# Kernel tuning notes

Hardware: AMD Instinct MI355X
Metric: run time of the kernel (lower is better)

The kernel has to match this reference:

```python
import jax, jax.numpy as jnp
import numpy as np

N_USER = 100000
N_RECIPE = 50000
E = 1000000
H = 128


def setup_inputs() -> dict:
    key = jax.random.key(0)
    ks = jax.random.split(key, 5)
    z_user = jax.random.normal(ks[0], (N_USER, H), dtype=jnp.float32)
    z_recipe = jax.random.normal(ks[1], (N_RECIPE, H), dtype=jnp.float32)
    edge_label_index = jax.random.randint(ks[2], (2, E), 0, N_RECIPE, dtype=jnp.int64)
    W1 = jax.random.normal(ks[3], (2 * H, H), dtype=jnp.float32) * (1.0 / np.sqrt(2 * H))
    b1 = jnp.zeros((H,), dtype=jnp.float32)
    W2 = jax.random.normal(ks[4], (H, 1), dtype=jnp.float32) * (1.0 / np.sqrt(H))
    b2 = jnp.zeros((1,), dtype=jnp.float32)
    return {"z_user": z_user, "z_recipe": z_recipe,
            "edge_label_index": edge_label_index,
            "W1": W1, "b1": b1, "W2": W2, "b2": b2}


def reference(z_user, z_recipe, edge_label_index, W1, b1, W2, b2):
    row, col = edge_label_index[0], edge_label_index[1]
    # gather + concat: [E, 2H]
    z = jnp.concatenate([z_user[row], z_recipe[col]], axis=-1)
    h = jax.nn.relu(z @ W1 + b1)        # [E, H]
    out = h @ W2 + b2                    # [E, 1]
    return out.reshape(-1)
```

## Files before the change

kernel.cpp:

```cpp
#include <hip/hip_runtime.h>
#include <hip/hip_bf16.h>


#define HDIM 128

typedef __attribute__((ext_vector_type(8))) __bf16 bf16x8;
typedef __attribute__((ext_vector_type(16))) float f32x16;

static __device__ __forceinline__ unsigned short bf16_bits(float x) {
  return __builtin_bit_cast(unsigned short, static_cast<__bf16>(x));
}

static __device__ __forceinline__ float bf2f(unsigned short u) {
  return __builtin_bit_cast(float, ((unsigned int)u) << 16);
}

static __device__ __forceinline__ bf16x8 cvt8(float4 a, float4 b) {
  bf16x8 r;
  r[0] = static_cast<__bf16>(a.x);
  r[1] = static_cast<__bf16>(a.y);
  r[2] = static_cast<__bf16>(a.z);
  r[3] = static_cast<__bf16>(a.w);
  r[4] = static_cast<__bf16>(b.x);
  r[5] = static_cast<__bf16>(b.y);
  r[6] = static_cast<__bf16>(b.z);
  r[7] = static_cast<__bf16>(b.w);
  return r;
}

__global__ void prep_w1(const float* __restrict__ W1,
                        unsigned short* __restrict__ W1bf) {
  const int tid = threadIdx.x;
#pragma unroll
  for (int it = 0; it < 8; ++it) {
    const int idx = (blockIdx.x << 11) + (it << 8) + tid;
    const int k = idx >> 7;
    const int n = idx & 127;
    const int kc = k >> 4;
    const int q = (k >> 3) & 1;
    const int j = k & 7;
    const int nt = n >> 5;
    const int ln = (q << 5) | (n & 31);
    W1bf[((((kc << 2) + nt) << 6) | ln) * 8 + j] = bf16_bits(W1[idx]);
  }
}

__global__ __launch_bounds__(256, 4) void proj_nodes(
    const float* __restrict__ zu, int NU, const float* __restrict__ zr, int NR,
    const float* __restrict__ W1, const unsigned short* __restrict__ W1bf,
    unsigned short* __restrict__ Hu, unsigned short* __restrict__ Hr,
    int ublocks) {
  __shared__ unsigned short Bsw[16384];
  const int tid = threadIdx.x;
  const bool isU = (int)blockIdx.x < ublocks;
  const int kc0 = isU ? 0 : 8;

  if (W1bf) {
    const uint4* s4 = (const uint4*)(W1bf + (kc0 << 11));
    uint4* d4 = (uint4*)Bsw;
#pragma unroll
    for (int i = 0; i < 8; ++i) d4[(i << 8) + tid] = s4[(i << 8) + tid];
  } else {
    const int n = tid & 127;
    const int kh = tid >> 7;
    const int nt = n >> 5;
    const int nl = n & 31;
#pragma unroll 8
    for (int it = 0; it < 64; ++it) {
      const int kl = 2 * it + kh;
      const float w = W1[(kc0 * 16 + kl) * HDIM + n];
      const int kc = kl >> 4;
      const int q = (kl >> 3) & 1;
      const int j = kl & 7;
      const int ln = (q << 5) | nl;
      Bsw[((((kc << 2) + nt) << 6) | ln) * 8 + j] = bf16_bits(w);
    }
  }
  __syncthreads();

  const int lane = tid & 63;
  const int wid = tid >> 6;
  const int m = lane & 31;
  const int half = lane >> 5;
  const int koff = half * 8;

  const int tl = (isU ? (int)blockIdx.x : (int)blockIdx.x - ublocks) * 4 + wid;
  const int ntype = isU ? ((NU + 31) >> 5) : ((NR + 31) >> 5);
  if (tl >= ntype) return;

  const int base = tl << 5;
  const int nmax = isU ? NU : NR;
  int node = base + m;
  if (node >= nmax) node = nmax - 1;
  const float* src = (isU ? zu : zr) + (size_t)node * HDIM + koff;

  f32x16 acc[4];
#pragma unroll
  for (int nt = 0; nt < 4; ++nt) acc[nt] = (f32x16)0.0f;

#pragma unroll
  for (int kcl = 0; kcl < 8; ++kcl) {
    const float4* sa = (const float4*)(src + kcl * 16);
    const bf16x8 a = cvt8(sa[0], sa[1]);
#pragma unroll
    for (int nt = 0; nt < 4; ++nt) {
      const uint4* bp =
          (const uint4*)(Bsw + ((((kcl << 2) + nt) << 6) | lane) * 8);
      const bf16x8 bfr = __builtin_bit_cast(bf16x8, *bp);
      acc[nt] = __builtin_amdgcn_mfma_f32_32x32x16_bf16(a, bfr, acc[nt], 0, 0, 0);
    }
  }

  unsigned short* H = isU ? Hu : Hr;
#pragma unroll
  for (int nt = 0; nt < 4; ++nt) {
#pragma unroll
    for (int r = 0; r < 16; ++r) {
      const int row = (r & 3) + ((r >> 2) << 3) + (half << 2);
      const int nrow = base + row;
      if (nrow < nmax)
        H[(size_t)nrow * HDIM + (nt << 5) + m] = bf16_bits(acc[nt][r]);
    }
  }
}

static __device__ __forceinline__ float dot8(uint4 a, uint4 b,
                                             const float* b1c,
                                             const float* w2c) {
  const unsigned short* pa = (const unsigned short*)&a;
  const unsigned short* pb = (const unsigned short*)&b;
  float s = 0.f;
#pragma unroll
  for (int j = 0; j < 8; ++j) {
    const float h = bf2f(pa[j]) + bf2f(pb[j]) + b1c[j];
    s = fmaf(fmaxf(h, 0.f), w2c[j], s);
  }
  return s;
}

__global__ __launch_bounds__(256, 4) void edge_pass(
    const unsigned short* __restrict__ Hu, const unsigned short* __restrict__ Hr,
    const int* __restrict__ eidx, const float* __restrict__ b1,
    const float* __restrict__ W2, const float* __restrict__ b2,
    float* __restrict__ out, int E) {
  const int tid = threadIdx.x;
  const int lane = tid & 63;
  const int c = lane & 15;
  const int g = lane >> 4;
  const int wid = blockIdx.x * 4 + (tid >> 6);
  const int stride = gridDim.x * 4 * 16;

  float b1c[8], w2c[8];
#pragma unroll
  for (int j = 0; j < 8; ++j) {
    b1c[j] = b1[c * 8 + j];
    w2c[j] = W2[c * 8 + j];
  }
  const float b2v = b2[0];
  const int co = c * 8;

  int e = wid * 16 + g * 4;
  if (e >= E) return;
  int iu0 = eidx[e],     ir0 = eidx[E + e];
  int iu1 = eidx[e + 1], ir1 = eidx[E + e + 1];
  int iu2 = eidx[e + 2], ir2 = eidx[E + e + 2];
  int iu3 = eidx[e + 3], ir3 = eidx[E + e + 3];

  while (true) {
    const int en = e + stride;
    const bool more = en < E;
    const int ep = more ? en : e;

    const uint4 au0 = *(const uint4*)(Hu + (size_t)iu0 * HDIM + co);
    const uint4 ar0 = *(const uint4*)(Hr + (size_t)ir0 * HDIM + co);
    const uint4 au1 = *(const uint4*)(Hu + (size_t)iu1 * HDIM + co);
    const uint4 ar1 = *(const uint4*)(Hr + (size_t)ir1 * HDIM + co);
    const uint4 au2 = *(const uint4*)(Hu + (size_t)iu2 * HDIM + co);
    const uint4 ar2 = *(const uint4*)(Hr + (size_t)ir2 * HDIM + co);
    const uint4 au3 = *(const uint4*)(Hu + (size_t)iu3 * HDIM + co);
    const uint4 ar3 = *(const uint4*)(Hr + (size_t)ir3 * HDIM + co);

    const int niu0 = eidx[ep],     nir0 = eidx[E + ep];
    const int niu1 = eidx[ep + 1], nir1 = eidx[E + ep + 1];
    const int niu2 = eidx[ep + 2], nir2 = eidx[E + ep + 2];
    const int niu3 = eidx[ep + 3], nir3 = eidx[E + ep + 3];

    float s0 = dot8(au0, ar0, b1c, w2c);
    float s1 = dot8(au1, ar1, b1c, w2c);
    float s2 = dot8(au2, ar2, b1c, w2c);
    float s3 = dot8(au3, ar3, b1c, w2c);
#pragma unroll
    for (int st = 1; st <= 8; st <<= 1) {
      s0 += __shfl_xor(s0, st);
      s1 += __shfl_xor(s1, st);
      s2 += __shfl_xor(s2, st);
      s3 += __shfl_xor(s3, st);
    }
    if (c == 0) {
      out[e]     = s0 + b2v;
      out[e + 1] = s1 + b2v;
      out[e + 2] = s2 + b2v;
      out[e + 3] = s3 + b2v;
    }
    if (!more) break;
    e = en;
    iu0 = niu0; ir0 = nir0; iu1 = niu1; ir1 = nir1;
    iu2 = niu2; ir2 = nir2; iu3 = niu3; ir3 = nir3;
  }
}

__global__ __launch_bounds__(256, 2) void edge_decoder_mfma(
    const float* __restrict__ zu, const float* __restrict__ zr,
    const int* __restrict__ eidx, const float* __restrict__ W1,
    const float* __restrict__ b1, const float* __restrict__ W2,
    const float* __restrict__ b2, float* __restrict__ out, int E) {
  __shared__ unsigned short Bsw[32768];
  const int tid = threadIdx.x;
  {
    const int n = tid & 127;
    const int kh = tid >> 7;
    const int nt = n >> 5;
    const int nl = n & 31;
#pragma unroll 8
    for (int it = 0; it < 128; ++it) {
      const int k = 2 * it + kh;
      const float w = W1[k * HDIM + n];
      const int kc = k >> 4;
      const int q = (k >> 3) & 1;
      const int j = k & 7;
      const int ln = (q << 5) | nl;
      Bsw[((((kc << 2) + nt) << 6) | ln) * 8 + j] = bf16_bits(w);
    }
  }
  __syncthreads();

  const int lane = tid & 63;
  const int wid = tid >> 6;
  const int m = lane & 31;
  const int half = lane >> 5;
  const int nsweep = E >> 6;
  const int wstride = gridDim.x * 4;

  float b1v[4], w2v[4];
#pragma unroll
  for (int nt = 0; nt < 4; ++nt) {
    b1v[nt] = b1[nt * 32 + m];
    w2v[nt] = W2[nt * 32 + m];
  }
  const float b2v = b2[0];
  const int koff = half * 8;

  for (int s = blockIdx.x * 4 + wid; s < nsweep; s += wstride) {
    const int e0 = s << 6;
    const int eA = e0 + m;
    const int eB = e0 + 32 + m;
    const float* puA = zu + (size_t)eidx[eA] * HDIM;
    const float* prA = zr + (size_t)eidx[E + eA] * HDIM;
    const float* puB = zu + (size_t)eidx[eB] * HDIM;
    const float* prB = zr + (size_t)eidx[E + eB] * HDIM;

    f32x16 acc[2][4];
#pragma unroll
    for (int mt = 0; mt < 2; ++mt)
#pragma unroll
      for (int nt = 0; nt < 4; ++nt) acc[mt][nt] = (f32x16)0.0f;

#pragma unroll
    for (int kc = 0; kc < 16; ++kc) {
      const float* srcA = (kc < 8) ? (puA + kc * 16 + koff) : (prA + (kc - 8) * 16 + koff);
      const float* srcB = (kc < 8) ? (puB + kc * 16 + koff) : (prB + (kc - 8) * 16 + koff);
      const float4* sa = (const float4*)srcA;
      const float4* sb = (const float4*)srcB;
      const bf16x8 a0 = cvt8(sa[0], sa[1]);
      const bf16x8 a1 = cvt8(sb[0], sb[1]);
#pragma unroll
      for (int nt = 0; nt < 4; ++nt) {
        const uint4* bp = (const uint4*)(Bsw + ((((kc << 2) + nt) << 6) | lane) * 8);
        const bf16x8 bfr = __builtin_bit_cast(bf16x8, *bp);
        acc[0][nt] = __builtin_amdgcn_mfma_f32_32x32x16_bf16(a0, bfr, acc[0][nt], 0, 0, 0);
        acc[1][nt] = __builtin_amdgcn_mfma_f32_32x32x16_bf16(a1, bfr, acc[1][nt], 0, 0, 0);
      }
    }

    float p0[16], p1[16];
#pragma unroll
    for (int r = 0; r < 16; ++r) { p0[r] = 0.f; p1[r] = 0.f; }
#pragma unroll
    for (int nt = 0; nt < 4; ++nt) {
#pragma unroll
      for (int r = 0; r < 16; ++r) {
        float h0 = fmaxf(acc[0][nt][r] + b1v[nt], 0.f);
        float h1 = fmaxf(acc[1][nt][r] + b1v[nt], 0.f);
        p0[r] = fmaf(h0, w2v[nt], p0[r]);
        p1[r] = fmaf(h1, w2v[nt], p1[r]);
      }
    }
#pragma unroll
    for (int st = 1; st <= 16; st <<= 1) {
#pragma unroll
      for (int r = 0; r < 16; ++r) {
        p0[r] += __shfl_xor(p0[r], st);
        p1[r] += __shfl_xor(p1[r], st);
      }
    }
    const int sel = lane & 15;
    const int mtw = (lane >> 4) & 1;
    float val = 0.f;
#pragma unroll
    for (int r = 0; r < 16; ++r) {
      const float cand = mtw ? p1[r] : p0[r];
      val = (sel == r) ? cand : val;
    }
    const int mrow = (sel & 3) + ((sel >> 2) << 3) + (half << 2);
    out[e0 + (mtw << 5) + mrow] = val + b2v;
  }
}

extern "C" void kernel_launch(void* const* d_in, const int* in_sizes, int n_in,
                              void* d_out, int out_size, void* d_ws,
                              size_t ws_size, hipStream_t stream) {
  const float* zu = (const float*)d_in[0];
  const float* zr = (const float*)d_in[1];
  const int* eidx = (const int*)d_in[2];
  const float* W1 = (const float*)d_in[3];
  const float* b1 = (const float*)d_in[4];
  const float* W2 = (const float*)d_in[5];
  const float* b2 = (const float*)d_in[6];
  float* out = (float*)d_out;
  const int nu = in_sizes[0];
  const int nr = in_sizes[1];
  const int E = in_sizes[2] / 2;
  const int NU = nu / HDIM, NR = nr / HDIM;

  const size_t needH = (size_t)(nu + nr) * sizeof(unsigned short);
  const size_t needW = 32768 * sizeof(unsigned short);

  if (ws_size >= needH) {
    unsigned short* Hu = (unsigned short*)d_ws;
    unsigned short* Hr = Hu + (size_t)nu;
    unsigned short* W1bf = nullptr;
    if (ws_size >= needH + needW) {
      W1bf = Hr + (size_t)nr;
      hipLaunchKernelGGL(prep_w1, dim3(16), dim3(256), 0, stream, W1, W1bf);
    }
    const int utiles = (NU + 31) >> 5;
    const int rtiles = (NR + 31) >> 5;
    const int ub = (utiles + 3) >> 2;
    const int rb = (rtiles + 3) >> 2;
    hipLaunchKernelGGL(proj_nodes, dim3(ub + rb), dim3(256), 0, stream,
                       zu, NU, zr, NR, W1, W1bf, Hu, Hr, ub);
    hipLaunchKernelGGL(edge_pass, dim3(2048), dim3(256), 0, stream,
                       Hu, Hr, eidx, b1, W2, b2, out, E);
  } else {
    hipLaunchKernelGGL(edge_decoder_mfma, dim3(512), dim3(256), 0, stream,
                       zu, zr, eidx, W1, b1, W2, b2, out, E);
  }
}
```

Before: 196.5 us.

## Skip projecting user nodes beyond max referenced row index; double edge grid

A merged prep kernel converts W1 to bf16 and also computes per-block maxima of the row indices. The node projection kernel reduces these maxima and skips user tiles whose base exceeds the largest referenced user index, avoiding projection work and reads for unreferenced users. The edge pass grid size is doubled. The extra scan of the row indices adds a small read pass before projection.

```diff
diff --git a/kernel.cpp b/kernel.cpp
--- a/kernel.cpp
+++ b/kernel.cpp
@@ -28,26 +28,45 @@
   return r;
 }
 
-__global__ void prep_w1(const float* __restrict__ W1,
-                        unsigned short* __restrict__ W1bf) {
+__global__ __launch_bounds__(256) void prep(const float* __restrict__ W1,
+                                            unsigned short* __restrict__ W1bf,
+                                            const int* __restrict__ eidx, int E,
+                                            int* __restrict__ maxarr) {
   const int tid = threadIdx.x;
-#pragma unroll
-  for (int it = 0; it < 8; ++it) {
-    const int idx = (blockIdx.x << 11) + (it << 8) + tid;
-    const int k = idx >> 7;
-    const int n = idx & 127;
-    const int kc = k >> 4;
-    const int q = (k >> 3) & 1;
-    const int j = k & 7;
-    const int nt = n >> 5;
-    const int ln = (q << 5) | (n & 31);
-    W1bf[((((kc << 2) + nt) << 6) | ln) * 8 + j] = bf16_bits(W1[idx]);
+  const int b = blockIdx.x;
+  if (b < 16 && W1bf) {
+#pragma unroll
+    for (int it = 0; it < 8; ++it) {
+      const int idx = (b << 11) + (it << 8) + tid;
+      const int k = idx >> 7;
+      const int n = idx & 127;
+      const int kc = k >> 4;
+      const int q = (k >> 3) & 1;
+      const int j = k & 7;
+      const int nt = n >> 5;
+      const int ln = (q << 5) | (n & 31);
+      W1bf[((((kc << 2) + nt) << 6) | ln) * 8 + j] = bf16_bits(W1[idx]);
+    }
+  }
+  int local = -1;
+  for (int i = b * 256 + tid; i < E; i += 64 * 256)
+    local = max(local, eidx[i]);
+#pragma unroll
+  for (int st = 1; st <= 32; st <<= 1)
+    local = max(local, __shfl_xor(local, st));
+  __shared__ int wmax[4];
+  if ((tid & 63) == 0) wmax[tid >> 6] = local;
+  __syncthreads();
+  if (tid == 0) {
+    int m = max(max(wmax[0], wmax[1]), max(wmax[2], wmax[3]));
+    maxarr[b] = m;
   }
 }
 
 __global__ __launch_bounds__(256, 4) void proj_nodes(
     const float* __restrict__ zu, int NU, const float* __restrict__ zr, int NR,
     const float* __restrict__ W1, const unsigned short* __restrict__ W1bf,
+    const int* __restrict__ maxarr,
     unsigned short* __restrict__ Hu, unsigned short* __restrict__ Hr,
     int ublocks) {
   __shared__ unsigned short Bsw[16384];
@@ -89,6 +108,14 @@
   if (tl >= ntype) return;
 
   const int base = tl << 5;
+
+  if (isU && maxarr) {
+    int v = maxarr[lane];
+#pragma unroll
+    for (int st = 1; st <= 32; st <<= 1) v = max(v, __shfl_xor(v, st));
+    if (base > v) return;
+  }
+
   const int nmax = isU ? NU : NR;
   int node = base + m;
   if (node >= nmax) node = nmax - 1;
@@ -334,22 +361,26 @@
 
   const size_t needH = (size_t)(nu + nr) * sizeof(unsigned short);
   const size_t needW = 32768 * sizeof(unsigned short);
+  const size_t needM = 64 * sizeof(int);
 
   if (ws_size >= needH) {
     unsigned short* Hu = (unsigned short*)d_ws;
     unsigned short* Hr = Hu + (size_t)nu;
     unsigned short* W1bf = nullptr;
-    if (ws_size >= needH + needW) {
+    int* maxarr = nullptr;
+    if (ws_size >= needH + needW + needM) {
       W1bf = Hr + (size_t)nr;
-      hipLaunchKernelGGL(prep_w1, dim3(16), dim3(256), 0, stream, W1, W1bf);
+      maxarr = (int*)(W1bf + 32768);
+      hipLaunchKernelGGL(prep, dim3(64), dim3(256), 0, stream,
+                         W1, W1bf, eidx, E, maxarr);
     }
     const int utiles = (NU + 31) >> 5;
     const int rtiles = (NR + 31) >> 5;
     const int ub = (utiles + 3) >> 2;
     const int rb = (rtiles + 3) >> 2;
     hipLaunchKernelGGL(proj_nodes, dim3(ub + rb), dim3(256), 0, stream,
-                       zu, NU, zr, NR, W1, W1bf, Hu, Hr, ub);
-    hipLaunchKernelGGL(edge_pass, dim3(2048), dim3(256), 0, stream,
+                       zu, NU, zr, NR, W1, W1bf, maxarr, Hu, Hr, ub);
+    hipLaunchKernelGGL(edge_pass, dim3(4096), dim3(256), 0, stream,
                        Hu, Hr, eidx, b1, W2, b2, out, E);
   } else {
     hipLaunchKernelGGL(edge_decoder_mfma, dim3(512), dim3(256), 0, stream,
```

New measurement: 192.6 us. 1.02x faster.
